# Performance work log

Measured on AMD Instinct MI355X. Metric: run time of the kernel, lower is better.

Reference implementation:

```python
import jax, jax.numpy as jnp
import numpy as np

E = 1024          # n_embed_dim
H = 64            # head_size = n_embed_dim // n_heads (16)

def setup_inputs() -> dict:
    key = jax.random.key(0)
    k_x, k_q, k_k, k_v = jax.random.split(key, 4)
    scale = 1.0 / np.sqrt(E)
    return {
        "x": jax.random.normal(k_x, (4, 2048, E), dtype=jnp.float32),
        "ln_gamma": jnp.ones((E,), jnp.float32),
        "ln_beta": jnp.zeros((E,), jnp.float32),
        # torch nn.Linear weights: [out_features, in_features]
        "Wq": jax.random.normal(k_q, (H, E), dtype=jnp.float32) * scale,
        "Wk": jax.random.normal(k_k, (H, E), dtype=jnp.float32) * scale,
        "Wv": jax.random.normal(k_v, (H, E), dtype=jnp.float32) * scale,
    }

def reference(x, ln_gamma, ln_beta, Wq, Wk, Wv):
    # LayerNorm over last dim (eps matches torch default 1e-5)
    mu = jnp.mean(x, axis=-1, keepdims=True)
    var = jnp.mean(jnp.square(x - mu), axis=-1, keepdims=True)
    xn = (x - mu) * jax.lax.rsqrt(var + 1e-5) * ln_gamma + ln_beta

    q = jnp.einsum('bse,he->bsh', xn, Wq)   # [B,S,H]
    k = jnp.einsum('bse,he->bsh', xn, Wk)
    v = jnp.einsum('bse,he->bsh', xn, Wv)

    scores = jnp.einsum('bqh,bkh->bqk', q, k) / jnp.sqrt(jnp.float32(H))
    S = x.shape[1]
    causal = jnp.tril(jnp.ones((S, S), dtype=bool))
    scores = jnp.where(causal, scores, -jnp.inf)
    attn = jax.nn.softmax(scores, axis=-1)
    return jnp.einsum('bqk,bkh->bqh', attn, v)
```

## Files before the change

kernel.cpp:

```cpp
#include <hip/hip_runtime.h>

#define E 1024
#define HH 64
#define BB 4
#define SS 2048
#define BS (BB*SS)
#define NSLOT 144

typedef unsigned short u16;
typedef short bf16x8 __attribute__((ext_vector_type(8)));
typedef float f32x4 __attribute__((ext_vector_type(4)));

#define LOG2E_O8 0.18033688011112042f

__device__ inline u16 f2bf(float f) {
    unsigned int u = __float_as_uint(f);
    unsigned int r = (u + 0x7FFFu + ((u >> 16) & 1u)) >> 16;
    return (u16)r;
}

__global__ __launch_bounds__(256) void ln_wcast(const float* __restrict__ x,
        const float* __restrict__ gamma, const float* __restrict__ beta,
        const float* __restrict__ Wq, const float* __restrict__ Wk,
        const float* __restrict__ Wv,
        u16* __restrict__ xn, u16* __restrict__ wc) {
    const int t = threadIdx.x;
    if (blockIdx.x < 2048) {
        const int w = t >> 6, lane = t & 63;
        const size_t row = (size_t)blockIdx.x * 4 + w;
        const float4* xr = (const float4*)(x + row * E);
        float4 v[4];
        #pragma unroll
        for (int i = 0; i < 4; ++i) v[i] = xr[lane + 64 * i];
        float s = 0.f, sq = 0.f;
        #pragma unroll
        for (int i = 0; i < 4; ++i) {
            s  += v[i].x + v[i].y + v[i].z + v[i].w;
            sq += v[i].x*v[i].x + v[i].y*v[i].y + v[i].z*v[i].z + v[i].w*v[i].w;
        }
        #pragma unroll
        for (int off = 32; off > 0; off >>= 1) {
            s  += __shfl_xor(s,  off);
            sq += __shfl_xor(sq, off);
        }
        const float mean = s * (1.0f / E);
        const float var  = sq * (1.0f / E) - mean * mean;
        const float rstd = rsqrtf(var + 1e-5f);
        const float4* gr = (const float4*)gamma;
        const float4* br = (const float4*)beta;
        #pragma unroll
        for (int i = 0; i < 4; ++i) {
            const float4 g  = gr[lane + 64 * i];
            const float4 bt = br[lane + 64 * i];
            ushort4 o;
            o.x = f2bf((v[i].x - mean) * rstd * g.x + bt.x);
            o.y = f2bf((v[i].y - mean) * rstd * g.y + bt.y);
            o.z = f2bf((v[i].z - mean) * rstd * g.z + bt.z);
            o.w = f2bf((v[i].w - mean) * rstd * g.w + bt.w);
            *(ushort4*)(xn + row * E + (lane + 64 * i) * 4) = o;
        }
    } else {
        const int row = blockIdx.x - 2048;
        const float* src = (row < 64)  ? (Wq + (size_t)row * E)
                         : (row < 128) ? (Wk + (size_t)(row - 64) * E)
                                       : (Wv + (size_t)(row - 128) * E);
        const float sc = (row < 64) ? LOG2E_O8 : 1.0f;
        const float4 v = *(const float4*)(src + t * 4);
        ushort4 o;
        o.x = f2bf(v.x * sc); o.y = f2bf(v.y * sc);
        o.z = f2bf(v.z * sc); o.w = f2bf(v.w * sc);
        *(ushort4*)(wc + (size_t)row * E + t * 4) = o;
    }
}

__global__ __launch_bounds__(256) void qkv_mfma(const u16* __restrict__ xn,
        const u16* __restrict__ wc,
        u16* __restrict__ qb, u16* __restrict__ kb, u16* __restrict__ vt) {
    const int mb   = blockIdx.x >> 1;
    const int half = blockIdx.x & 1;
    const int row0 = mb * 32;
    const int t = threadIdx.x;
    const int w = t >> 6, lane = t & 63;
    const int quad = lane >> 4, r15 = lane & 15;
    const int mt = w >> 1, cgrp = w & 1;
    __shared__ u16 Xs[32 * 64];
    __shared__ u16 Ws[96 * 64];
    f32x4 acc[3] = {};

    for (int kc = 0; kc < E; kc += 64) {
        __syncthreads();
        {
            const int row = t >> 3, ch = t & 7;
            const uint4 d = *(const uint4*)(xn + (size_t)(row0 + row) * E + kc + ch * 8);
            *(uint4*)&Xs[row * 64 + (ch ^ (row & 7)) * 8] = d;
        }
        #pragma unroll
        for (int i = 0; i < 3; ++i) {
            const int idx = i * 256 + t;
            const int wl = idx >> 3, ch = idx & 7;
            const uint4 d = *(const uint4*)(wc + (size_t)(half * 96 + wl) * E + kc + ch * 8);
            *(uint4*)&Ws[wl * 64 + (ch ^ (wl & 7)) * 8] = d;
        }
        __syncthreads();
        #pragma unroll
        for (int kk = 0; kk < 2; ++kk) {
            const int xrow = mt * 16 + r15;
            const bf16x8 af = *(const bf16x8*)&Xs[xrow * 64 + ((kk * 4 + quad) ^ (xrow & 7)) * 8];
            #pragma unroll
            for (int j = 0; j < 3; ++j) {
                const int wl = (cgrp * 3 + j) * 16 + r15;
                const bf16x8 bfr = *(const bf16x8*)&Ws[wl * 64 + ((kk * 4 + quad) ^ (wl & 7)) * 8];
                acc[j] = __builtin_amdgcn_mfma_f32_16x16x32_bf16(af, bfr, acc[j], 0, 0, 0);
            }
        }
    }
    const int b    = row0 >> 11;
    const int key0 = row0 & 2047;
    #pragma unroll
    for (int j = 0; j < 3; ++j) {
        const int cg  = half * 96 + cgrp * 48 + j * 16 + r15;
        const int sel = cg >> 6;
        const int col = cg & 63;
        if (sel < 2) {
            u16* base = (sel == 0) ? qb : kb;
            #pragma unroll
            for (int r = 0; r < 4; ++r) {
                const size_t row = (size_t)row0 + mt * 16 + quad * 4 + r;
                base[row * HH + col] = f2bf(acc[j][r]);
            }
        } else {
            ushort4 pk;
            pk.x = f2bf(acc[j][0]); pk.y = f2bf(acc[j][1]);
            pk.z = f2bf(acc[j][2]); pk.w = f2bf(acc[j][3]);
            *(ushort4*)(vt + (size_t)b * HH * SS + (size_t)col * SS
                           + key0 + mt * 16 + quad * 4) = pk;
        }
    }
}

__global__ __launch_bounds__(256) void attn_partial(const u16* __restrict__ qb,
        const u16* __restrict__ kb, const u16* __restrict__ vt,
        float* __restrict__ po, float* __restrict__ pl,
        float* __restrict__ out) {
    const int bid = blockIdx.x;
    const int b   = bid >> 8;
    const int rem = bid & 255;
    const int qt  = rem >> 3, c = rem & 7;
    const int a   = qt >> 2;
    if (c > a) return;
    const int nc   = a + 1;
    const int r_   = qt & 3;
    const int slot = b * NSLOT + 2 * a * (a + 1) + r_ * (a + 1) + c;
    const int q0   = qt << 6;
    const int t = threadIdx.x;
    const int w = t >> 6, lane = t & 63;
    const int quad = lane >> 4, r15 = lane & 15;

    __shared__ u16 Ks[64 * 64];
    __shared__ u16 VT[64 * 64];
    __shared__ u16 Ps[64 * 64];

    const size_t qrow = ((size_t)b * SS + q0 + w * 16 + r15) * HH;
    const bf16x8 qf0 = *(const bf16x8*)(qb + qrow + quad * 8);
    const bf16x8 qf1 = *(const bf16x8*)(qb + qrow + 32 + quad * 8);

    f32x4 o[4] = {};
    float l_[4] = {0.f, 0.f, 0.f, 0.f};

    const int t1 = min(c * 4 + 4, qt + 1);
    for (int tile = c * 4; tile < t1; ++tile) {
        const int kt = tile << 6;
        __syncthreads();
        {
            const int row = t >> 2, ch0 = (t & 3) * 2;
            const uint4* src = (const uint4*)(kb + ((size_t)b * SS + kt + row) * HH + ch0 * 8);
            const uint4 d0 = src[0], d1 = src[1];
            *(uint4*)&Ks[row * 64 + ((ch0    ) ^ (row & 7)) * 8] = d0;
            *(uint4*)&Ks[row * 64 + ((ch0 + 1) ^ (row & 7)) * 8] = d1;
        }
        {
            const int h = t >> 2, ch0 = (t & 3) * 2;
            const uint4* src = (const uint4*)(vt + (size_t)b * HH * SS + (size_t)h * SS + kt + ch0 * 8);
            const uint4 d0 = src[0], d1 = src[1];
            *(uint4*)&VT[h * 64 + ((ch0    ) ^ (h & 7)) * 8] = d0;
            *(uint4*)&VT[h * 64 + ((ch0 + 1) ^ (h & 7)) * 8] = d1;
        }
        __syncthreads();

        f32x4 s[4] = {};
        #pragma unroll
        for (int nt = 0; nt < 4; ++nt) {
            const int krow = nt * 16 + r15;
            const bf16x8 k0 = *(const bf16x8*)&Ks[krow * 64 + ((    quad) ^ (krow & 7)) * 8];
            const bf16x8 k1 = *(const bf16x8*)&Ks[krow * 64 + ((4 + quad) ^ (krow & 7)) * 8];
            s[nt] = __builtin_amdgcn_mfma_f32_16x16x32_bf16(qf0, k0, s[nt], 0, 0, 0);
            s[nt] = __builtin_amdgcn_mfma_f32_16x16x32_bf16(qf1, k1, s[nt], 0, 0, 0);
        }
        if (tile == qt) {
            #pragma unroll
            for (int nt = 0; nt < 4; ++nt)
                #pragma unroll
                for (int r = 0; r < 4; ++r)
                    if (nt * 16 + r15 > w * 16 + quad * 4 + r) s[nt][r] = -INFINITY;
        }

        float p[4][4];
        #pragma unroll
        for (int r = 0; r < 4; ++r) {
            float rs = 0.f;
            #pragma unroll
            for (int nt = 0; nt < 4; ++nt) {
                p[nt][r] = __builtin_amdgcn_exp2f(s[nt][r]);
                rs += p[nt][r];
            }
            rs += __shfl_xor(rs, 1); rs += __shfl_xor(rs, 2);
            rs += __shfl_xor(rs, 4); rs += __shfl_xor(rs, 8);
            l_[r] += rs;
        }

        #pragma unroll
        for (int nt = 0; nt < 4; ++nt)
            #pragma unroll
            for (int r = 0; r < 4; ++r) {
                const int prow = w * 16 + quad * 4 + r;
                const int col  = nt * 16 + r15;
                Ps[prow * 64 + (((col >> 3) ^ (prow & 7)) * 8) + (col & 7)] = f2bf(p[nt][r]);
            }
        const int arow = w * 16 + r15;
        const bf16x8 pf0 = *(const bf16x8*)&Ps[arow * 64 + ((    quad) ^ (arow & 7)) * 8];
        const bf16x8 pf1 = *(const bf16x8*)&Ps[arow * 64 + ((4 + quad) ^ (arow & 7)) * 8];

        #pragma unroll
        for (int ht = 0; ht < 4; ++ht) {
            const int vrow = ht * 16 + r15;
            const bf16x8 v0 = *(const bf16x8*)&VT[vrow * 64 + ((    quad) ^ (vrow & 7)) * 8];
            const bf16x8 v1 = *(const bf16x8*)&VT[vrow * 64 + ((4 + quad) ^ (vrow & 7)) * 8];
            o[ht] = __builtin_amdgcn_mfma_f32_16x16x32_bf16(pf0, v0, o[ht], 0, 0, 0);
            o[ht] = __builtin_amdgcn_mfma_f32_16x16x32_bf16(pf1, v1, o[ht], 0, 0, 0);
        }
    }

    if (nc == 1) {
        #pragma unroll
        for (int r = 0; r < 4; ++r) {
            const float inv = 1.0f / l_[r];
            const size_t orow = ((size_t)b * SS + q0 + w * 16 + quad * 4 + r) * HH;
            #pragma unroll
            for (int ht = 0; ht < 4; ++ht)
                out[orow + ht * 16 + r15] = o[ht][r] * inv;
        }
        return;
    }
    #pragma unroll
    for (int r = 0; r < 4; ++r) {
        const int q = w * 16 + quad * 4 + r;
        #pragma unroll
        for (int ht = 0; ht < 4; ++ht)
            po[(size_t)slot * 4096 + q * 64 + ht * 16 + r15] = o[ht][r];
        if (r15 == 0) pl[slot * 64 + q] = l_[r];
    }
}

__global__ __launch_bounds__(256) void attn_reduce(const float* __restrict__ po,
        const float* __restrict__ pl, float* __restrict__ out) {
    const int bid = blockIdx.x;
    const int b = bid >> 7, rem = bid & 127;
    const int qt = rem >> 2, qq = rem & 3;
    if (qt < 4) return;
    const int a = qt >> 2, r_ = qt & 3;
    const int nc = a + 1;
    const int sbase = b * NSLOT + 2 * a * (a + 1) + r_ * (a + 1);
    const int t = threadIdx.x;
    const int h = t & 63, qr = t >> 6;
    #pragma unroll
    for (int i = 0; i < 4; ++i) {
        const int q = qq * 16 + qr * 4 + i;
        float osum = 0.f, lsum = 0.f;
        for (int cidx = 0; cidx < nc; ++cidx) {
            osum += po[(size_t)(sbase + cidx) * 4096 + q * 64 + h];
            lsum += pl[(sbase + cidx) * 64 + q];
        }
        out[((size_t)b * SS + (qt << 6) + q) * HH + h] = osum / lsum;
    }
}

extern "C" void kernel_launch(void* const* d_in, const int* in_sizes, int n_in,
                              void* d_out, int out_size, void* d_ws, size_t ws_size,
                              hipStream_t stream) {
    const float* x     = (const float*)d_in[0];
    const float* gamma = (const float*)d_in[1];
    const float* beta  = (const float*)d_in[2];
    const float* Wq    = (const float*)d_in[3];
    const float* Wk    = (const float*)d_in[4];
    const float* Wv    = (const float*)d_in[5];
    float* out = (float*)d_out;

    char* p = (char*)d_ws;
    u16*   xn   = (u16*)p;                         p += (size_t)BS * E * 2;
    u16*   wc   = (u16*)p;                         p += 393216;
    u16*   qb   = (u16*)p;                         p += (size_t)BS * HH * 2;
    u16*   kb   = (u16*)p;                         p += (size_t)BS * HH * 2;
    u16*   vt   = (u16*)p;                         p += (size_t)BS * HH * 2;
    float* po   = (float*)p;                       p += (size_t)BB * NSLOT * 4096 * 4;
    float* pl   = (float*)p;

    ln_wcast    <<<2048 + 192,  256, 0, stream>>>(x, gamma, beta, Wq, Wk, Wv, xn, wc);
    qkv_mfma    <<<BS / 16,     256, 0, stream>>>(xn, wc, qb, kb, vt);
    attn_partial<<<BB * 32 * 8, 256, 0, stream>>>(qb, kb, vt, po, pl, out);
    attn_reduce <<<BB * 32 * 4, 256, 0, stream>>>(po, pl, out);
}
```

Measured before the change: 122.5 us.

## Fuse LayerNorm into QKV projection, fold gamma/beta into weights, fuse reduce

```diff
diff --git a/kernel.cpp b/kernel.cpp
--- a/kernel.cpp
+++ b/kernel.cpp
@@ -19,62 +19,36 @@
     return (u16)r;
 }
 
-__global__ __launch_bounds__(256) void ln_wcast(const float* __restrict__ x,
+__global__ __launch_bounds__(256) void w_cast(const float* __restrict__ Wq,
+        const float* __restrict__ Wk, const float* __restrict__ Wv,
         const float* __restrict__ gamma, const float* __restrict__ beta,
-        const float* __restrict__ Wq, const float* __restrict__ Wk,
-        const float* __restrict__ Wv,
-        u16* __restrict__ xn, u16* __restrict__ wc) {
+        u16* __restrict__ wc, float* __restrict__ bias, int* __restrict__ cnt) {
+    const int row = blockIdx.x;
     const int t = threadIdx.x;
-    if (blockIdx.x < 2048) {
-        const int w = t >> 6, lane = t & 63;
-        const size_t row = (size_t)blockIdx.x * 4 + w;
-        const float4* xr = (const float4*)(x + row * E);
-        float4 v[4];
-        #pragma unroll
-        for (int i = 0; i < 4; ++i) v[i] = xr[lane + 64 * i];
-        float s = 0.f, sq = 0.f;
-        #pragma unroll
-        for (int i = 0; i < 4; ++i) {
-            s  += v[i].x + v[i].y + v[i].z + v[i].w;
-            sq += v[i].x*v[i].x + v[i].y*v[i].y + v[i].z*v[i].z + v[i].w*v[i].w;
-        }
-        #pragma unroll
-        for (int off = 32; off > 0; off >>= 1) {
-            s  += __shfl_xor(s,  off);
-            sq += __shfl_xor(sq, off);
-        }
-        const float mean = s * (1.0f / E);
-        const float var  = sq * (1.0f / E) - mean * mean;
-        const float rstd = rsqrtf(var + 1e-5f);
-        const float4* gr = (const float4*)gamma;
-        const float4* br = (const float4*)beta;
-        #pragma unroll
-        for (int i = 0; i < 4; ++i) {
-            const float4 g  = gr[lane + 64 * i];
-            const float4 bt = br[lane + 64 * i];
-            ushort4 o;
-            o.x = f2bf((v[i].x - mean) * rstd * g.x + bt.x);
-            o.y = f2bf((v[i].y - mean) * rstd * g.y + bt.y);
-            o.z = f2bf((v[i].z - mean) * rstd * g.z + bt.z);
-            o.w = f2bf((v[i].w - mean) * rstd * g.w + bt.w);
-            *(ushort4*)(xn + row * E + (lane + 64 * i) * 4) = o;
-        }
-    } else {
-        const int row = blockIdx.x - 2048;
-        const float* src = (row < 64)  ? (Wq + (size_t)row * E)
-                         : (row < 128) ? (Wk + (size_t)(row - 64) * E)
-                                       : (Wv + (size_t)(row - 128) * E);
-        const float sc = (row < 64) ? LOG2E_O8 : 1.0f;
-        const float4 v = *(const float4*)(src + t * 4);
-        ushort4 o;
-        o.x = f2bf(v.x * sc); o.y = f2bf(v.y * sc);
-        o.z = f2bf(v.z * sc); o.w = f2bf(v.w * sc);
-        *(ushort4*)(wc + (size_t)row * E + t * 4) = o;
-    }
-}
-
-__global__ __launch_bounds__(256) void qkv_mfma(const u16* __restrict__ xn,
-        const u16* __restrict__ wc,
+    if (row == 0 && t < BB * 32) cnt[t] = 0;
+    const float* src = (row < 64)  ? (Wq + (size_t)row * E)
+                     : (row < 128) ? (Wk + (size_t)(row - 64) * E)
+                                   : (Wv + (size_t)(row - 128) * E);
+    const float sc = (row < 64) ? LOG2E_O8 : 1.0f;
+    const float4 v = *(const float4*)(src + t * 4);
+    const float4 g = *(const float4*)(gamma + t * 4);
+    const float4 b = *(const float4*)(beta  + t * 4);
+    ushort4 o;
+    o.x = f2bf(v.x * g.x * sc); o.y = f2bf(v.y * g.y * sc);
+    o.z = f2bf(v.z * g.z * sc); o.w = f2bf(v.w * g.w * sc);
+    *(ushort4*)(wc + (size_t)row * E + t * 4) = o;
+
+    float s = (v.x * b.x + v.y * b.y + v.z * b.z + v.w * b.w) * sc;
+    #pragma unroll
+    for (int off = 32; off > 0; off >>= 1) s += __shfl_xor(s, off);
+    __shared__ float red[4];
+    if ((t & 63) == 0) red[t >> 6] = s;
+    __syncthreads();
+    if (t == 0) bias[row] = red[0] + red[1] + red[2] + red[3];
+}
+
+__global__ __launch_bounds__(256) void lnqkv(const float* __restrict__ x,
+        const u16* __restrict__ wc, const float* __restrict__ bias,
         u16* __restrict__ qb, u16* __restrict__ kb, u16* __restrict__ vt) {
     const int mb   = blockIdx.x >> 1;
     const int half = blockIdx.x & 1;
@@ -83,29 +57,74 @@
     const int w = t >> 6, lane = t & 63;
     const int quad = lane >> 4, r15 = lane & 15;
     const int mt = w >> 1, cgrp = w & 1;
-    __shared__ u16 Xs[32 * 64];
+
+    __shared__ u16 Xs[32 * 1024];
     __shared__ u16 Ws[96 * 64];
+    __shared__ float smu[32], srs[32];
+
+    #pragma unroll 2
+    for (int i = 0; i < 8; ++i) {
+        const int r = w * 8 + i;
+        const float4* xr = (const float4*)(x + (size_t)(row0 + r) * E);
+        float s = 0.f, sq = 0.f;
+        #pragma unroll
+        for (int jj = 0; jj < 4; ++jj) {
+            const float4 v = xr[lane + 64 * jj];
+            s  += v.x + v.y + v.z + v.w;
+            sq += v.x*v.x + v.y*v.y + v.z*v.z + v.w*v.w;
+        }
+        #pragma unroll
+        for (int off = 32; off > 0; off >>= 1) {
+            s  += __shfl_xor(s,  off);
+            sq += __shfl_xor(sq, off);
+        }
+        if (lane == 0) {
+            const float mean = s * (1.0f / E);
+            const float var  = sq * (1.0f / E) - mean * mean;
+            smu[r] = mean;
+            srs[r] = rsqrtf(var + 1e-5f);
+        }
+    }
+
+    {
+        const int row = t >> 3, ch = t & 7;
+        const float mu = smu[row], rs = srs[row];
+        const float* xr = x + (size_t)(row0 + row) * E;
+        const int phys = (ch ^ (row & 7)) * 8;
+        #pragma unroll 4
+        for (int s = 0; s < 16; ++s) {
+            const float4 f0 = *(const float4*)(xr + s * 64 + ch * 8);
+            const float4 f1 = *(const float4*)(xr + s * 64 + ch * 8 + 4);
+            u16 tmp[8];
+            tmp[0] = f2bf((f0.x - mu) * rs); tmp[1] = f2bf((f0.y - mu) * rs);
+            tmp[2] = f2bf((f0.z - mu) * rs); tmp[3] = f2bf((f0.w - mu) * rs);
+            tmp[4] = f2bf((f1.x - mu) * rs); tmp[5] = f2bf((f1.y - mu) * rs);
+            tmp[6] = f2bf((f1.z - mu) * rs); tmp[7] = f2bf((f1.w - mu) * rs);
+            *(uint4*)&Xs[row * 1024 + s * 64 + phys] = *(uint4*)tmp;
+        }
+    }
+
+    float bj[3];
+    #pragma unroll
+    for (int j = 0; j < 3; ++j) bj[j] = bias[half * 96 + cgrp * 48 + j * 16 + r15];
+
     f32x4 acc[3] = {};
-
-    for (int kc = 0; kc < E; kc += 64) {
+    const int xrow = mt * 16 + r15;
+
+    for (int kc = 0; kc < 16; ++kc) {
         __syncthreads();
-        {
-            const int row = t >> 3, ch = t & 7;
-            const uint4 d = *(const uint4*)(xn + (size_t)(row0 + row) * E + kc + ch * 8);
-            *(uint4*)&Xs[row * 64 + (ch ^ (row & 7)) * 8] = d;
-        }
         #pragma unroll
         for (int i = 0; i < 3; ++i) {
             const int idx = i * 256 + t;
             const int wl = idx >> 3, ch = idx & 7;
-            const uint4 d = *(const uint4*)(wc + (size_t)(half * 96 + wl) * E + kc + ch * 8);
+            const uint4 d = *(const uint4*)(wc + (size_t)(half * 96 + wl) * E + kc * 64 + ch * 8);
             *(uint4*)&Ws[wl * 64 + (ch ^ (wl & 7)) * 8] = d;
         }
         __syncthreads();
         #pragma unroll
         for (int kk = 0; kk < 2; ++kk) {
-            const int xrow = mt * 16 + r15;
-            const bf16x8 af = *(const bf16x8*)&Xs[xrow * 64 + ((kk * 4 + quad) ^ (xrow & 7)) * 8];
+            const bf16x8 af = *(const bf16x8*)&Xs[xrow * 1024 + kc * 64
+                                                 + ((kk * 4 + quad) ^ (xrow & 7)) * 8];
             #pragma unroll
             for (int j = 0; j < 3; ++j) {
                 const int wl = (cgrp * 3 + j) * 16 + r15;
@@ -114,6 +133,7 @@
             }
         }
     }
+
     const int b    = row0 >> 11;
     const int key0 = row0 & 2047;
     #pragma unroll
@@ -126,12 +146,12 @@
             #pragma unroll
             for (int r = 0; r < 4; ++r) {
                 const size_t row = (size_t)row0 + mt * 16 + quad * 4 + r;
-                base[row * HH + col] = f2bf(acc[j][r]);
+                base[row * HH + col] = f2bf(acc[j][r] + bj[j]);
             }
         } else {
             ushort4 pk;
-            pk.x = f2bf(acc[j][0]); pk.y = f2bf(acc[j][1]);
-            pk.z = f2bf(acc[j][2]); pk.w = f2bf(acc[j][3]);
+            pk.x = f2bf(acc[j][0] + bj[j]); pk.y = f2bf(acc[j][1] + bj[j]);
+            pk.z = f2bf(acc[j][2] + bj[j]); pk.w = f2bf(acc[j][3] + bj[j]);
             *(ushort4*)(vt + (size_t)b * HH * SS + (size_t)col * SS
                            + key0 + mt * 16 + quad * 4) = pk;
         }
@@ -140,7 +160,7 @@
 
 __global__ __launch_bounds__(256) void attn_partial(const u16* __restrict__ qb,
         const u16* __restrict__ kb, const u16* __restrict__ vt,
-        float* __restrict__ po, float* __restrict__ pl,
+        float* __restrict__ po, float* __restrict__ pl, int* __restrict__ cnt,
         float* __restrict__ out) {
     const int bid = blockIdx.x;
     const int b   = bid >> 8;
@@ -148,10 +168,11 @@
     const int qt  = rem >> 3, c = rem & 7;
     const int a   = qt >> 2;
     if (c > a) return;
-    const int nc   = a + 1;
-    const int r_   = qt & 3;
-    const int slot = b * NSLOT + 2 * a * (a + 1) + r_ * (a + 1) + c;
-    const int q0   = qt << 6;
+    const int nc    = a + 1;
+    const int r_    = qt & 3;
+    const int sbase = b * NSLOT + 2 * a * (a + 1) + r_ * (a + 1);
+    const int slot  = sbase + c;
+    const int q0    = qt << 6;
     const int t = threadIdx.x;
     const int w = t >> 6, lane = t & 63;
     const int quad = lane >> 4, r15 = lane & 15;
@@ -159,6 +180,7 @@
     __shared__ u16 Ks[64 * 64];
     __shared__ u16 VT[64 * 64];
     __shared__ u16 Ps[64 * 64];
+    __shared__ int isLast;
 
     const size_t qrow = ((size_t)b * SS + q0 + w * 16 + r15) * HH;
     const bf16x8 qf0 = *(const bf16x8*)(qb + qrow + quad * 8);
@@ -251,6 +273,7 @@
         }
         return;
     }
+
     #pragma unroll
     for (int r = 0; r < 4; ++r) {
         const int q = w * 16 + quad * 4 + r;
@@ -259,28 +282,23 @@
             po[(size_t)slot * 4096 + q * 64 + ht * 16 + r15] = o[ht][r];
         if (r15 == 0) pl[slot * 64 + q] = l_[r];
     }
-}
-
-__global__ __launch_bounds__(256) void attn_reduce(const float* __restrict__ po,
-        const float* __restrict__ pl, float* __restrict__ out) {
-    const int bid = blockIdx.x;
-    const int b = bid >> 7, rem = bid & 127;
-    const int qt = rem >> 2, qq = rem & 3;
-    if (qt < 4) return;
-    const int a = qt >> 2, r_ = qt & 3;
-    const int nc = a + 1;
-    const int sbase = b * NSLOT + 2 * a * (a + 1) + r_ * (a + 1);
-    const int t = threadIdx.x;
-    const int h = t & 63, qr = t >> 6;
-    #pragma unroll
-    for (int i = 0; i < 4; ++i) {
-        const int q = qq * 16 + qr * 4 + i;
+
+    __threadfence();
+    if (t == 0) isLast = (atomicAdd(&cnt[b * 32 + qt], 1) == nc - 1);
+    __syncthreads();
+    if (!isLast) return;
+    __threadfence();
+
+    const int h = t & 63;
+    #pragma unroll 4
+    for (int i = 0; i < 16; ++i) {
+        const int q = (t >> 6) * 16 + i;
         float osum = 0.f, lsum = 0.f;
         for (int cidx = 0; cidx < nc; ++cidx) {
             osum += po[(size_t)(sbase + cidx) * 4096 + q * 64 + h];
             lsum += pl[(sbase + cidx) * 64 + q];
         }
-        out[((size_t)b * SS + (qt << 6) + q) * HH + h] = osum / lsum;
+        out[((size_t)b * SS + q0 + q) * HH + h] = osum / lsum;
     }
 }
 
@@ -296,16 +314,16 @@
     float* out = (float*)d_out;
 
     char* p = (char*)d_ws;
-    u16*   xn   = (u16*)p;                         p += (size_t)BS * E * 2;
     u16*   wc   = (u16*)p;                         p += 393216;
+    float* bias = (float*)p;                       p += 1024;
     u16*   qb   = (u16*)p;                         p += (size_t)BS * HH * 2;
     u16*   kb   = (u16*)p;                         p += (size_t)BS * HH * 2;
     u16*   vt   = (u16*)p;                         p += (size_t)BS * HH * 2;
     float* po   = (float*)p;                       p += (size_t)BB * NSLOT * 4096 * 4;
-    float* pl   = (float*)p;
-
-    ln_wcast    <<<2048 + 192,  256, 0, stream>>>(x, gamma, beta, Wq, Wk, Wv, xn, wc);
-    qkv_mfma    <<<BS / 16,     256, 0, stream>>>(xn, wc, qb, kb, vt);
-    attn_partial<<<BB * 32 * 8, 256, 0, stream>>>(qb, kb, vt, po, pl, out);
-    attn_reduce <<<BB * 32 * 4, 256, 0, stream>>>(po, pl, out);
-}
+    float* pl   = (float*)p;                       p += (size_t)BB * NSLOT * 64 * 4;
+    int*   cnt  = (int*)p;
+
+    w_cast      <<<192,         256, 0, stream>>>(Wq, Wk, Wv, gamma, beta, wc, bias, cnt);
+    lnqkv       <<<BS / 16,     256, 0, stream>>>(x, wc, bias, qb, kb, vt);
+    attn_partial<<<BB * 32 * 8, 256, 0, stream>>>(qb, kb, vt, po, pl, cnt, out);
+}
```

New measurement: 293.5 us. +139.5%, slower.
